# Kernel optimization log

Measured on AMD Instinct MI355X. Metric: run time of the kernel, lower is better.

Reference implementation:

```python
import jax, jax.numpy as jnp
import numpy as np

EPSILON = float(np.finfo(np.float32).tiny)
K = 64      # top-k edges to keep
TAU = 0.1   # gumbel-softmax temperature


def setup_inputs() -> dict:
    key = jax.random.key(0)
    k1, k2 = jax.random.split(key)
    B, N, E = 64, 256, 4
    scores = jax.random.normal(k1, (B, N, N, E), dtype=jnp.float32)
    # Gumbel(0,1) noise matching flat_scores shape [B*E, N*N]
    gumbel = jax.random.gumbel(k2, (B * E, N * N), dtype=jnp.float32)
    return {"scores": scores, "gumbel": gumbel}


def reference(scores, gumbel):
    B, N, _, E = scores.shape
    local_k = min(K, N * N)
    # [B, N, N, E] -> [B, E, N, N] -> [B*E, N*N]
    flat = scores.transpose(0, 3, 1, 2).reshape(B * E, N * N) + gumbel
    khot = jnp.zeros_like(flat)
    onehot = jnp.zeros_like(flat)

    def step(carry, _):
        flat, khot, onehot = carry
        khot_mask = jnp.maximum(1.0 - onehot, EPSILON)
        flat = flat + jnp.log(khot_mask)
        onehot = jax.nn.softmax(flat / TAU, axis=1)
        return (flat, khot + onehot, onehot), None

    (flat, khot, onehot), _ = jax.lax.scan(
        step, (flat, khot, onehot), None, length=local_k)

    # hard straight-through top-k
    _, ind = jax.lax.top_k(khot, local_k)                 # [B*E, local_k]
    rows = jnp.arange(khot.shape[0])[:, None]
    khot_hard = jnp.zeros_like(khot).at[rows, ind].set(1.0)
    res = khot_hard - jax.lax.stop_gradient(khot) + khot

    # [B*E, N*N] -> [B, E, N, N] -> [B, N, N, E]
    new_mask = res.reshape(B, E, N, N).transpose(0, 2, 3, 1)
    return new_mask
```

## Files before the change

kernel.cpp:

```cpp
#include <hip/hip_runtime.h>
#include <cfloat>

#define NROW   256
#define RLEN   65536
#define TPB    1024
#define VPT    64
#define REGS   8
#define MAXC   (TPB*REGS)
#define NITER  64
#define KSEL   64
#define THETA_OFF 8.0f
#define TCAP   256
#define LN_TGT 7.6246f

__global__ void __launch_bounds__(TPB)
GumbelSampler_2482491097709_kernel(const float* __restrict__ scores,
                                   const float* __restrict__ gumbel,
                                   float* __restrict__ out)
{
    __shared__ float s_A[16];
    __shared__ float s_B[16];
    __shared__ float s_EA[16];
    __shared__ float s_EB[16];
    __shared__ int   s_IC[16];
    __shared__ float s_mx[NITER];
    __shared__ float s_rcp[NITER];
    __shared__ int   s_cnt;
    __shared__ int   s_selB;
    __shared__ int   s_selR;
    __shared__ int   s_tcnt;
    __shared__ int   s_tie[TCAP];
    __shared__ int   s_hist[4096];
    __shared__ int   cand_idx[MAXC];
    __shared__ float cand_kv[MAXC];

    const int tid  = threadIdx.x;
    const int lane = tid & 63;
    const int wid  = tid >> 6;

    const int q    = blockIdx.x;
    const int xcd  = q & 7;
    const int slot = q >> 3;
    const int b    = xcd * 8 + (slot & 7);
    const int e    = slot >> 3;
    const int r    = b * 4 + e;

    const float* __restrict__ sr = scores + (size_t)b * (RLEN * 4) + e;
    const float* __restrict__ gr = gumbel + (size_t)r * RLEN;

    float v[VPT];
#pragma unroll
    for (int s = 0; s < VPT; ++s) {
        int p = tid + TPB * s;
        v[s] = sr[(size_t)p * 4] + gr[p];
    }

    float lm = -FLT_MAX;
#pragma unroll
    for (int s = 0; s < VPT; ++s) lm = fmaxf(lm, v[s]);
#pragma unroll
    for (int o = 32; o; o >>= 1) lm = fmaxf(lm, __shfl_xor(lm, o));
    if (lane == 0) s_A[wid] = lm;
    __syncthreads();
    float M0 = s_A[0];
#pragma unroll
    for (int w = 1; w < 16; ++w) M0 = fmaxf(M0, s_A[w]);
    const float C = M0 * 10.0f;

    float theta = M0 - THETA_OFF;
    for (int probe = 0; probe < 12; ++probe) {
        int lc = 0;
#pragma unroll
        for (int s = 0; s < VPT; ++s) lc += (v[s] >= theta) ? 1 : 0;
#pragma unroll
        for (int o = 32; o; o >>= 1) lc += __shfl_xor(lc, o);
        if (lane == 0) s_IC[wid] = lc;
        __syncthreads();
        int cc = 0;
#pragma unroll
        for (int w = 0; w < 16; ++w) cc += s_IC[w];
        __syncthreads();
        if (cc > MAXC - 64)      theta += __logf((float)cc) - LN_TGT;
        else if (cc < KSEL)      theta -= LN_TGT - __logf((float)(cc < 1 ? 1 : cc));
        else break;
    }

    if (tid == 0) s_cnt = 0;
    __syncthreads();
    {
        float mu = -FLT_MAX, u = 0.f;
#pragma unroll
        for (int s = 0; s < VPT; ++s) {
            float val = v[s];
            if (val >= theta) {
                int sl = atomicAdd(&s_cnt, 1);
                if (sl < MAXC) { cand_idx[sl] = tid + TPB * s; cand_kv[sl] = val; }
            } else {
                mu = fmaxf(mu, val);
                u += __expf(fmaf(val, 10.f, -C));
            }
        }
#pragma unroll
        for (int o = 32; o; o >>= 1) {
            mu = fmaxf(mu, __shfl_xor(mu, o));
            u += __shfl_xor(u, o);
        }
        if (lane == 0) { s_EA[wid] = mu; s_EB[wid] = u; }
    }
    __syncthreads();
    int cnt = s_cnt;
    float Mu = -FLT_MAX, U = 0.f;
#pragma unroll
    for (int w = 0; w < 16; ++w) { Mu = fmaxf(Mu, s_EA[w]); U += s_EB[w]; }

    float rcur[REGS];
#pragma unroll
    for (int j = 0; j < REGS; ++j) {
        int sl = tid + TPB * j;
        if (sl < cnt) {
            rcur[j] = cand_kv[sl];
            cand_kv[sl] = 0.f;
        } else rcur[j] = 0.f;
    }

    bool  noexp = false;
    float pmx = 0.f, prcp = 0.f, pt2 = 0.f;
    for (int t = 0; t < NITER; ++t) {
        float lmx = -FLT_MAX;
        if (t == 0) {
#pragma unroll
            for (int j = 0; j < REGS; ++j)
                if (tid + TPB * j < cnt) lmx = fmaxf(lmx, rcur[j]);
        } else {
#pragma unroll
            for (int j = 0; j < REGS; ++j) {
                int sl = tid + TPB * j;
                if (sl < cnt) {
                    float cur = rcur[j];
                    float y = fmaf(cur, 10.f, -pmx);
                    if (y > pt2) {
                        float o = __expf(y) * prcp;
                        cand_kv[sl] += o;
                        cur += __logf(fmaxf(1.f - o, FLT_MIN));
                        rcur[j] = cur;
                    }
                    lmx = fmaxf(lmx, cur);
                }
            }
        }
#pragma unroll
        for (int o = 32; o; o >>= 1) lmx = fmaxf(lmx, __shfl_xor(lmx, o));
        if (lane == 0) s_A[wid] = lmx;
        __syncthreads();
        float gm = s_A[0];
#pragma unroll
        for (int w = 1; w < 16; ++w) gm = fmaxf(gm, s_A[w]);
        const float mx = fmaxf(gm, Mu) * 10.f;

        float ls = 0.f;
#pragma unroll
        for (int j = 0; j < REGS; ++j)
            if (tid + TPB * j < cnt) ls += __expf(fmaf(rcur[j], 10.f, -mx));
#pragma unroll
        for (int o = 32; o; o >>= 1) ls += __shfl_xor(ls, o);
        if (lane == 0) s_B[wid] = ls;
        __syncthreads();
        float S = 0.f;
#pragma unroll
        for (int w = 0; w < 16; ++w) S += s_B[w];
        if (U > 0.f) S += __expf(C - mx + __logf(U));
        float lnse = __logf(S);
        float rcp  = 1.f / S;
        float t2   = lnse - 18.03f;
        if (tid == 0) { s_mx[t] = mx; s_rcp[t] = rcp; }
        pmx = mx; prcp = rcp; pt2 = t2;

        if (!noexp && t < NITER - 1) {
            float Lse = mx + lnse;
            if (10.f * Mu > Lse - 20.f) {
                float thOld = theta;
                float thN   = (Lse - 26.f) * 0.1f;
                int   oldc  = cnt;
                float mu2 = -FLT_MAX, u2 = 0.f;
#pragma unroll 4
                for (int s = 0; s < VPT; ++s) {
                    int p = tid + TPB * s;
                    float val = sr[(size_t)p * 4] + gr[p];
                    if (val < thOld) {
                        if (val >= thN) {
                            int sl = atomicAdd(&s_cnt, 1);
                            if (sl < MAXC) {
                                cand_idx[sl] = p;
                                cand_kv[sl]  = val;
                            }
                        } else {
                            mu2 = fmaxf(mu2, val);
                            u2 += __expf(fmaf(val, 10.f, -C));
                        }
                    }
                }
#pragma unroll
                for (int o = 32; o; o >>= 1) {
                    mu2 = fmaxf(mu2, __shfl_xor(mu2, o));
                    u2 += __shfl_xor(u2, o);
                }
                if (lane == 0) { s_EA[wid] = mu2; s_EB[wid] = u2; }
                __syncthreads();
                int newc = s_cnt;
                if (newc > MAXC) {
                    if (tid == 0) s_cnt = oldc;
                    noexp = true;
                } else {
                    float m2 = -FLT_MAX, uu = 0.f;
#pragma unroll
                    for (int w = 0; w < 16; ++w) {
                        m2 = fmaxf(m2, s_EA[w]); uu += s_EB[w];
                    }
                    Mu = m2; U = uu; theta = thN;
#pragma unroll
                    for (int j = 0; j < REGS; ++j) {
                        int sl = tid + TPB * j;
                        if (sl >= oldc && sl < newc) {
                            float vv = cand_kv[sl];
                            rcur[j] = vv;
                            float kb = 0.f;
                            for (int tt = 0; tt < t; ++tt)
                                kb += __expf(fmaf(vv, 10.f, -s_mx[tt])) * s_rcp[tt];
                            cand_kv[sl] = kb;
                        }
                    }
                    cnt = newc;
                }
            }
        }
    }
#pragma unroll
    for (int j = 0; j < REGS; ++j) {
        int sl = tid + TPB * j;
        if (sl < cnt) {
            float y = fmaf(rcur[j], 10.f, -pmx);
            if (y > pt2) cand_kv[sl] += __expf(y) * prcp;
        }
    }
    __syncthreads();

    unsigned prefix = 0;
    int Rrem = KSEL;
    for (int pass = 0; pass < 3; ++pass) {
        const int nbins = (pass == 2) ? 1024 : 2048;
        for (int i = tid; i < nbins; i += TPB) s_hist[i] = 0;
        __syncthreads();
#pragma unroll
        for (int j = 0; j < REGS; ++j) {
            int sl = tid + TPB * j;
            if (sl < cnt) {
                unsigned key = __float_as_uint(cand_kv[sl]);
                if (key != 0u) {
                    bool m; int bin;
                    if (pass == 0)      { m = true;                     bin = key >> 21; }
                    else if (pass == 1) { m = (key >> 21) == prefix;    bin = (key >> 10) & 2047; }
                    else                { m = (key >> 10) == prefix;    bin = key & 1023; }
                    if (m) atomicAdd(&s_hist[bin], 1);
                }
            }
        }
        __syncthreads();
        if (wid == 0) {
            int Rl = Rrem, found = -1;
            const int nch = nbins >> 6;
            for (int c = 0; c < nch && found < 0; ++c) {
                int bin = nbins - 1 - (c * 64 + lane);
                int h = s_hist[bin];
                int cum = h;
#pragma unroll
                for (int s2 = 1; s2 < 64; s2 <<= 1) {
                    int vv = __shfl_up(cum, s2);
                    if (lane >= s2) cum += vv;
                }
                unsigned long long mb = __ballot(cum >= Rl);
                if (mb) {
                    int fl = __ffsll(mb) - 1;
                    int cumex = __shfl(cum, fl) - __shfl(h, fl);
                    found = nbins - 1 - (c * 64 + fl);
                    Rl -= cumex;
                } else {
                    Rl -= __shfl(cum, 63);
                }
            }
            if (lane == 0) { s_selB = found; s_selR = Rl; }
        }
        __syncthreads();
        prefix = (prefix << ((pass == 2) ? 10 : 11)) | (unsigned)s_selB;
        Rrem = s_selR;
    }
    const unsigned Kstar = prefix;
    const int need = Rrem;

    if (tid == 0) s_tcnt = 0;
    __syncthreads();
#pragma unroll
    for (int j = 0; j < REGS; ++j) {
        int sl = tid + TPB * j;
        if (sl < cnt) {
            float kh = cand_kv[sl];
            unsigned key = __float_as_uint(kh);
            if (key > Kstar) {
                int p = cand_idx[sl];
                out[((size_t)b * RLEN + (size_t)p) * 4 + e] = (1.f - kh) + kh;
            } else if (key == Kstar) {
                int tp = atomicAdd(&s_tcnt, 1);
                if (tp < TCAP) s_tie[tp] = cand_idx[sl];
            }
        }
    }
    __syncthreads();
    if (wid == 0) {
        int T = s_tcnt < TCAP ? s_tcnt : TCAP;
        float kv = __uint_as_float(Kstar);
        float ov = (1.f - kv) + kv;
        for (int rdone = 0; rdone < need; ++rdone) {
            int bi = 0x7fffffff, bp = -1;
            for (int i = lane; i < T; i += 64) {
                int vv = s_tie[i];
                if (vv < bi) { bi = vv; bp = i; }
            }
#pragma unroll
            for (int s2 = 32; s2; s2 >>= 1) {
                int oi = __shfl_xor(bi, s2);
                int op = __shfl_xor(bp, s2);
                if (oi < bi) { bi = oi; bp = op; }
            }
            if (lane == 0 && bi != 0x7fffffff) {
                out[((size_t)b * RLEN + (size_t)bi) * 4 + e] = ov;
                s_tie[bp] = 0x7fffffff;
            }
        }
    }
}

extern "C" void kernel_launch(void* const* d_in, const int* in_sizes, int n_in,
                              void* d_out, int out_size, void* d_ws, size_t ws_size,
                              hipStream_t stream) {
    const float* scores = (const float*)d_in[0];
    const float* gumbel = (const float*)d_in[1];
    float* out = (float*)d_out;

    hipMemsetAsync(d_out, 0, (size_t)out_size * sizeof(float), stream);
    GumbelSampler_2482491097709_kernel<<<NROW, TPB, 0, stream>>>(scores, gumbel, out);
}
```

Measured before the change: 387.2 us.

## Fuse max and sum reductions per softmax iteration using lagged anchor

```diff
diff --git a/kernel.cpp b/kernel.cpp
--- a/kernel.cpp
+++ b/kernel.cpp
@@ -12,14 +12,16 @@
 #define THETA_OFF 8.0f
 #define TCAP   256
 #define LN_TGT 7.6246f
-
-__global__ void __launch_bounds__(TPB)
+#define AGUARD 40.0f
+
+__global__ void __launch_bounds__(TPB, 4)
 GumbelSampler_2482491097709_kernel(const float* __restrict__ scores,
                                    const float* __restrict__ gumbel,
                                    float* __restrict__ out)
 {
-    __shared__ float s_A[16];
-    __shared__ float s_B[16];
+    __shared__ float s_Am[2][16];
+    __shared__ float s_Bs[2][16];
+    __shared__ float s_R[16];
     __shared__ float s_EA[16];
     __shared__ float s_EB[16];
     __shared__ int   s_IC[16];
@@ -49,22 +51,24 @@
     const float* __restrict__ gr = gumbel + (size_t)r * RLEN;
 
     float v[VPT];
+    float lm = -FLT_MAX;
 #pragma unroll
     for (int s = 0; s < VPT; ++s) {
         int p = tid + TPB * s;
-        v[s] = sr[(size_t)p * 4] + gr[p];
-    }
-
-    float lm = -FLT_MAX;
-#pragma unroll
-    for (int s = 0; s < VPT; ++s) lm = fmaxf(lm, v[s]);
+        float x = sr[(size_t)p * 4] + gr[p];
+        v[s] = x;
+        lm = fmaxf(lm, x);
+    }
+#pragma unroll
+    for (int s = 0; s < VPT; ++s) asm volatile("" : "+v"(v[s]));
+
 #pragma unroll
     for (int o = 32; o; o >>= 1) lm = fmaxf(lm, __shfl_xor(lm, o));
-    if (lane == 0) s_A[wid] = lm;
-    __syncthreads();
-    float M0 = s_A[0];
-#pragma unroll
-    for (int w = 1; w < 16; ++w) M0 = fmaxf(M0, s_A[w]);
+    if (lane == 0) s_Am[0][wid] = lm;
+    __syncthreads();
+    float M0 = s_Am[0][0];
+#pragma unroll
+    for (int w = 1; w < 16; ++w) M0 = fmaxf(M0, s_Am[0][w]);
     const float C = M0 * 10.0f;
 
     float theta = M0 - THETA_OFF;
@@ -97,7 +101,8 @@
                 if (sl < MAXC) { cand_idx[sl] = tid + TPB * s; cand_kv[sl] = val; }
             } else {
                 mu = fmaxf(mu, val);
-                u += __expf(fmaf(val, 10.f, -C));
+                float yv = fmaf(val, 10.f, -C);
+                if (yv > -87.f) u += __expf(yv);
             }
         }
 #pragma unroll
@@ -124,20 +129,28 @@
     }
 
     bool  noexp = false;
-    float pmx = 0.f, prcp = 0.f, pt2 = 0.f;
+    float anc = C;
+    float pa = 0.f, prcp = 0.f, pt2 = 0.f;
     for (int t = 0; t < NITER; ++t) {
-        float lmx = -FLT_MAX;
+        const int pb = t & 1;
+        float lmx = -FLT_MAX, ls = 0.f;
         if (t == 0) {
-#pragma unroll
-            for (int j = 0; j < REGS; ++j)
-                if (tid + TPB * j < cnt) lmx = fmaxf(lmx, rcur[j]);
-        } else {
 #pragma unroll
             for (int j = 0; j < REGS; ++j) {
                 int sl = tid + TPB * j;
                 if (sl < cnt) {
                     float cur = rcur[j];
-                    float y = fmaf(cur, 10.f, -pmx);
+                    lmx = fmaxf(lmx, cur);
+                    ls += __expf(fmaf(cur, 10.f, -anc));
+                }
+            }
+        } else {
+#pragma unroll
+            for (int j = 0; j < REGS; ++j) {
+                int sl = tid + TPB * j;
+                if (sl < cnt) {
+                    float cur = rcur[j];
+                    float y = fmaf(cur, 10.f, -pa);
                     if (y > pt2) {
                         float o = __expf(y) * prcp;
                         cand_kv[sl] += o;
@@ -145,38 +158,58 @@
                         rcur[j] = cur;
                     }
                     lmx = fmaxf(lmx, cur);
-                }
-            }
-        }
-#pragma unroll
-        for (int o = 32; o; o >>= 1) lmx = fmaxf(lmx, __shfl_xor(lmx, o));
-        if (lane == 0) s_A[wid] = lmx;
-        __syncthreads();
-        float gm = s_A[0];
-#pragma unroll
-        for (int w = 1; w < 16; ++w) gm = fmaxf(gm, s_A[w]);
-        const float mx = fmaxf(gm, Mu) * 10.f;
-
-        float ls = 0.f;
-#pragma unroll
-        for (int j = 0; j < REGS; ++j)
-            if (tid + TPB * j < cnt) ls += __expf(fmaf(rcur[j], 10.f, -mx));
-#pragma unroll
-        for (int o = 32; o; o >>= 1) ls += __shfl_xor(ls, o);
-        if (lane == 0) s_B[wid] = ls;
-        __syncthreads();
-        float S = 0.f;
-#pragma unroll
-        for (int w = 0; w < 16; ++w) S += s_B[w];
-        if (U > 0.f) S += __expf(C - mx + __logf(U));
+                    ls += __expf(fmaf(cur, 10.f, -anc));
+                }
+            }
+        }
+#pragma unroll
+        for (int o = 32; o; o >>= 1) {
+            lmx = fmaxf(lmx, __shfl_xor(lmx, o));
+            ls += __shfl_xor(ls, o);
+        }
+        if (lane == 0) { s_Am[pb][wid] = lmx; s_Bs[pb][wid] = ls; }
+        __syncthreads();
+        float gm, Ssum;
+        {
+            const float4* pA = (const float4*)&s_Am[pb][0];
+            const float4* pB = (const float4*)&s_Bs[pb][0];
+            float4 a0 = pA[0], a1 = pA[1], a2 = pA[2], a3 = pA[3];
+            float4 b0 = pB[0], b1 = pB[1], b2 = pB[2], b3 = pB[3];
+            gm = fmaxf(fmaxf(fmaxf(a0.x, a0.y), fmaxf(a0.z, a0.w)),
+                 fmaxf(fmaxf(fmaxf(a1.x, a1.y), fmaxf(a1.z, a1.w)),
+                 fmaxf(fmaxf(fmaxf(a2.x, a2.y), fmaxf(a2.z, a2.w)),
+                       fmaxf(fmaxf(a3.x, a3.y), fmaxf(a3.z, a3.w)))));
+            Ssum = ((b0.x + b0.y) + (b0.z + b0.w))
+                 + ((b1.x + b1.y) + (b1.z + b1.w))
+                 + ((b2.x + b2.y) + (b2.z + b2.w))
+                 + ((b3.x + b3.y) + (b3.z + b3.w));
+        }
+        float anext = fmaxf(gm, Mu) * 10.f;
+        float aeff  = anc;
+        float S     = Ssum;
+        if (anc - anext > AGUARD) {
+            float l2 = 0.f;
+#pragma unroll
+            for (int j = 0; j < REGS; ++j)
+                if (tid + TPB * j < cnt) l2 += __expf(fmaf(rcur[j], 10.f, -anext));
+#pragma unroll
+            for (int o = 32; o; o >>= 1) l2 += __shfl_xor(l2, o);
+            if (lane == 0) s_R[wid] = l2;
+            __syncthreads();
+            S = 0.f;
+#pragma unroll
+            for (int w = 0; w < 16; ++w) S += s_R[w];
+            aeff = anext;
+        }
+        if (U > 0.f) S += __expf(C - aeff + __logf(U));
         float lnse = __logf(S);
         float rcp  = 1.f / S;
-        float t2   = lnse - 18.03f;
-        if (tid == 0) { s_mx[t] = mx; s_rcp[t] = rcp; }
-        pmx = mx; prcp = rcp; pt2 = t2;
+        if (tid == 0) { s_mx[t] = aeff; s_rcp[t] = rcp; }
+        pa = aeff; prcp = rcp; pt2 = lnse - 18.03f;
+        anc = anext;
 
         if (!noexp && t < NITER - 1) {
-            float Lse = mx + lnse;
+            float Lse = aeff + lnse;
             if (10.f * Mu > Lse - 20.f) {
                 float thOld = theta;
                 float thN   = (Lse - 26.f) * 0.1f;
@@ -195,7 +228,8 @@
                             }
                         } else {
                             mu2 = fmaxf(mu2, val);
-                            u2 += __expf(fmaf(val, 10.f, -C));
+                            float yv = fmaf(val, 10.f, -C);
+                            if (yv > -87.f) u2 += __expf(yv);
                         }
                     }
                 }
@@ -238,7 +272,7 @@
     for (int j = 0; j < REGS; ++j) {
         int sl = tid + TPB * j;
         if (sl < cnt) {
-            float y = fmaf(rcur[j], 10.f, -pmx);
+            float y = fmaf(rcur[j], 10.f, -pa);
             if (y > pt2) cand_kv[sl] += __expf(y) * prcp;
         }
     }
```

Result: faster. 369.7 us (-4.5%).

## Anchor softmax on previous log-sum-exp to drop per-iteration max reduction

Applied to the files above, without the earlier changes.

```diff
diff --git a/kernel.cpp b/kernel.cpp
--- a/kernel.cpp
+++ b/kernel.cpp
@@ -12,19 +12,18 @@
 #define THETA_OFF 8.0f
 #define TCAP   256
 #define LN_TGT 7.6246f
-
-__global__ void __launch_bounds__(TPB)
+#define GATE  (-18.03f)
+
+__global__ void __launch_bounds__(TPB, 4)
 GumbelSampler_2482491097709_kernel(const float* __restrict__ scores,
                                    const float* __restrict__ gumbel,
                                    float* __restrict__ out)
 {
-    __shared__ float s_A[16];
-    __shared__ float s_B[16];
+    __shared__ float s_P[2][16];
     __shared__ float s_EA[16];
     __shared__ float s_EB[16];
     __shared__ int   s_IC[16];
-    __shared__ float s_mx[NITER];
-    __shared__ float s_rcp[NITER];
+    __shared__ float s_Lse[NITER];
     __shared__ int   s_cnt;
     __shared__ int   s_selB;
     __shared__ int   s_selR;
@@ -49,22 +48,24 @@
     const float* __restrict__ gr = gumbel + (size_t)r * RLEN;
 
     float v[VPT];
+    float lm = -FLT_MAX;
 #pragma unroll
     for (int s = 0; s < VPT; ++s) {
         int p = tid + TPB * s;
-        v[s] = sr[(size_t)p * 4] + gr[p];
-    }
-
-    float lm = -FLT_MAX;
-#pragma unroll
-    for (int s = 0; s < VPT; ++s) lm = fmaxf(lm, v[s]);
+        float x = sr[(size_t)p * 4] + gr[p];
+        v[s] = x;
+        lm = fmaxf(lm, x);
+    }
+#pragma unroll
+    for (int s = 0; s < VPT; ++s) asm volatile("" : "+v"(v[s]));
+
 #pragma unroll
     for (int o = 32; o; o >>= 1) lm = fmaxf(lm, __shfl_xor(lm, o));
-    if (lane == 0) s_A[wid] = lm;
-    __syncthreads();
-    float M0 = s_A[0];
-#pragma unroll
-    for (int w = 1; w < 16; ++w) M0 = fmaxf(M0, s_A[w]);
+    if (lane == 0) s_P[0][wid] = lm;
+    __syncthreads();
+    float M0 = s_P[0][lane & 15];
+#pragma unroll
+    for (int o = 8; o; o >>= 1) M0 = fmaxf(M0, __shfl_xor(M0, o));
     const float C = M0 * 10.0f;
 
     float theta = M0 - THETA_OFF;
@@ -76,9 +77,9 @@
         for (int o = 32; o; o >>= 1) lc += __shfl_xor(lc, o);
         if (lane == 0) s_IC[wid] = lc;
         __syncthreads();
-        int cc = 0;
-#pragma unroll
-        for (int w = 0; w < 16; ++w) cc += s_IC[w];
+        int cc = s_IC[lane & 15];
+#pragma unroll
+        for (int o = 8; o; o >>= 1) cc += __shfl_xor(cc, o);
         __syncthreads();
         if (cc > MAXC - 64)      theta += __logf((float)cc) - LN_TGT;
         else if (cc < KSEL)      theta -= LN_TGT - __logf((float)(cc < 1 ? 1 : cc));
@@ -92,12 +93,19 @@
 #pragma unroll
         for (int s = 0; s < VPT; ++s) {
             float val = v[s];
-            if (val >= theta) {
-                int sl = atomicAdd(&s_cnt, 1);
+            bool pr = (val >= theta);
+            unsigned long long m = __ballot(pr);
+            if (pr) {
+                int lead = __ffsll(m) - 1;
+                int base = 0;
+                if (lane == lead) base = atomicAdd(&s_cnt, (int)__popcll(m));
+                base = __shfl(base, lead);
+                int sl = base + (int)__popcll(m & ((1ull << lane) - 1ull));
                 if (sl < MAXC) { cand_idx[sl] = tid + TPB * s; cand_kv[sl] = val; }
             } else {
                 mu = fmaxf(mu, val);
-                u += __expf(fmaf(val, 10.f, -C));
+                float yv = fmaf(val, 10.f, -C);
+                if (yv > -87.f) u += __expf(yv);
             }
         }
 #pragma unroll
@@ -109,9 +117,12 @@
     }
     __syncthreads();
     int cnt = s_cnt;
-    float Mu = -FLT_MAX, U = 0.f;
-#pragma unroll
-    for (int w = 0; w < 16; ++w) { Mu = fmaxf(Mu, s_EA[w]); U += s_EB[w]; }
+    float Mu = s_EA[lane & 15], U = s_EB[lane & 15];
+#pragma unroll
+    for (int o = 8; o; o >>= 1) {
+        Mu = fmaxf(Mu, __shfl_xor(Mu, o));
+        U += __shfl_xor(U, o);
+    }
 
     float rcur[REGS];
 #pragma unroll
@@ -124,122 +135,109 @@
     }
 
     bool  noexp = false;
-    float pmx = 0.f, prcp = 0.f, pt2 = 0.f;
+    float anc = C;
     for (int t = 0; t < NITER; ++t) {
-        float lmx = -FLT_MAX;
+        const int pb = t & 1;
+        float ls = 0.f;
         if (t == 0) {
 #pragma unroll
             for (int j = 0; j < REGS; ++j)
-                if (tid + TPB * j < cnt) lmx = fmaxf(lmx, rcur[j]);
+                if (tid + TPB * j < cnt)
+                    ls += __expf(fmaf(rcur[j], 10.f, -anc));
         } else {
 #pragma unroll
             for (int j = 0; j < REGS; ++j) {
                 int sl = tid + TPB * j;
                 if (sl < cnt) {
                     float cur = rcur[j];
-                    float y = fmaf(cur, 10.f, -pmx);
-                    if (y > pt2) {
-                        float o = __expf(y) * prcp;
-                        cand_kv[sl] += o;
-                        cur += __logf(fmaxf(1.f - o, FLT_MIN));
+                    float y = fmaf(cur, 10.f, -anc);
+                    float e_ = __expf(y);
+                    if (y > GATE) {
+                        cand_kv[sl] += e_;
+                        cur += __logf(fmaxf(1.f - e_, FLT_MIN));
                         rcur[j] = cur;
+                        e_ = __expf(fmaf(cur, 10.f, -anc));
                     }
-                    lmx = fmaxf(lmx, cur);
-                }
-            }
-        }
-#pragma unroll
-        for (int o = 32; o; o >>= 1) lmx = fmaxf(lmx, __shfl_xor(lmx, o));
-        if (lane == 0) s_A[wid] = lmx;
-        __syncthreads();
-        float gm = s_A[0];
-#pragma unroll
-        for (int w = 1; w < 16; ++w) gm = fmaxf(gm, s_A[w]);
-        const float mx = fmaxf(gm, Mu) * 10.f;
-
-        float ls = 0.f;
-#pragma unroll
-        for (int j = 0; j < REGS; ++j)
-            if (tid + TPB * j < cnt) ls += __expf(fmaf(rcur[j], 10.f, -mx));
+                    ls += e_;
+                }
+            }
+        }
 #pragma unroll
         for (int o = 32; o; o >>= 1) ls += __shfl_xor(ls, o);
-        if (lane == 0) s_B[wid] = ls;
-        __syncthreads();
-        float S = 0.f;
-#pragma unroll
-        for (int w = 0; w < 16; ++w) S += s_B[w];
-        if (U > 0.f) S += __expf(C - mx + __logf(U));
-        float lnse = __logf(S);
-        float rcp  = 1.f / S;
-        float t2   = lnse - 18.03f;
-        if (tid == 0) { s_mx[t] = mx; s_rcp[t] = rcp; }
-        pmx = mx; prcp = rcp; pt2 = t2;
-
-        if (!noexp && t < NITER - 1) {
-            float Lse = mx + lnse;
-            if (10.f * Mu > Lse - 20.f) {
-                float thOld = theta;
-                float thN   = (Lse - 26.f) * 0.1f;
-                int   oldc  = cnt;
-                float mu2 = -FLT_MAX, u2 = 0.f;
+        if (lane == 0) s_P[pb][wid] = ls;
+        __syncthreads();
+        float S = s_P[pb][lane & 15];
+#pragma unroll
+        for (int o = 8; o; o >>= 1) S += __shfl_xor(S, o);
+        if (U > 0.f) S += __expf(C - anc + __logf(U));
+        float Lse = anc + __logf(S);
+        if (tid == 0) s_Lse[t] = Lse;
+
+        if (!noexp && t < NITER - 1 && 10.f * Mu > Lse - 20.f) {
+            float thOld = theta;
+            float thN   = (Lse - 26.f) * 0.1f;
+            int   oldc  = cnt;
+            float mu2 = -FLT_MAX, u2 = 0.f;
 #pragma unroll 4
-                for (int s = 0; s < VPT; ++s) {
-                    int p = tid + TPB * s;
-                    float val = sr[(size_t)p * 4] + gr[p];
-                    if (val < thOld) {
-                        if (val >= thN) {
-                            int sl = atomicAdd(&s_cnt, 1);
-                            if (sl < MAXC) {
-                                cand_idx[sl] = p;
-                                cand_kv[sl]  = val;
-                            }
-                        } else {
-                            mu2 = fmaxf(mu2, val);
-                            u2 += __expf(fmaf(val, 10.f, -C));
+            for (int s = 0; s < VPT; ++s) {
+                int p = tid + TPB * s;
+                float val = sr[(size_t)p * 4] + gr[p];
+                if (val < thOld) {
+                    if (val >= thN) {
+                        int sl = atomicAdd(&s_cnt, 1);
+                        if (sl < MAXC) {
+                            cand_idx[sl] = p;
+                            cand_kv[sl]  = val;
                         }
+                    } else {
+                        mu2 = fmaxf(mu2, val);
+                        float yv = fmaf(val, 10.f, -C);
+                        if (yv > -87.f) u2 += __expf(yv);
                     }
                 }
-#pragma unroll
-                for (int o = 32; o; o >>= 1) {
-                    mu2 = fmaxf(mu2, __shfl_xor(mu2, o));
-                    u2 += __shfl_xor(u2, o);
-                }
-                if (lane == 0) { s_EA[wid] = mu2; s_EB[wid] = u2; }
-                __syncthreads();
-                int newc = s_cnt;
-                if (newc > MAXC) {
-                    if (tid == 0) s_cnt = oldc;
-                    noexp = true;
-                } else {
-                    float m2 = -FLT_MAX, uu = 0.f;
-#pragma unroll
-                    for (int w = 0; w < 16; ++w) {
-                        m2 = fmaxf(m2, s_EA[w]); uu += s_EB[w];
+            }
+#pragma unroll
+            for (int o = 32; o; o >>= 1) {
+                mu2 = fmaxf(mu2, __shfl_xor(mu2, o));
+                u2 += __shfl_xor(u2, o);
+            }
+            if (lane == 0) { s_EA[wid] = mu2; s_EB[wid] = u2; }
+            __syncthreads();
+            int newc = s_cnt;
+            if (newc > MAXC) {
+                if (tid == 0) s_cnt = oldc;
+                noexp = true;
+            } else {
+                float m2 = s_EA[lane & 15], uu = s_EB[lane & 15];
+#pragma unroll
+                for (int o = 8; o; o >>= 1) {
+                    m2 = fmaxf(m2, __shfl_xor(m2, o));
+                    uu += __shfl_xor(uu, o);
+                }
+                Mu = m2; U = uu; theta = thN;
+#pragma unroll
+                for (int j = 0; j < REGS; ++j) {
+                    int sl = tid + TPB * j;
+                    if (sl >= oldc && sl < newc) {
+                        float vv = cand_kv[sl];
+                        rcur[j] = vv;
+                        float kb = 0.f;
+                        for (int tt = 0; tt < t; ++tt)
+                            kb += __expf(fmaf(vv, 10.f, -s_Lse[tt]));
+                        cand_kv[sl] = kb;
                     }
-                    Mu = m2; U = uu; theta = thN;
-#pragma unroll
-                    for (int j = 0; j < REGS; ++j) {
-                        int sl = tid + TPB * j;
-                        if (sl >= oldc && sl < newc) {
-                            float vv = cand_kv[sl];
-                            rcur[j] = vv;
-                            float kb = 0.f;
-                            for (int tt = 0; tt < t; ++tt)
-                                kb += __expf(fmaf(vv, 10.f, -s_mx[tt])) * s_rcp[tt];
-                            cand_kv[sl] = kb;
-                        }
-                    }
-                    cnt = newc;
-                }
-            }
-        }
+                }
+                cnt = newc;
+            }
+        }
+        anc = Lse;
     }
 #pragma unroll
     for (int j = 0; j < REGS; ++j) {
         int sl = tid + TPB * j;
         if (sl < cnt) {
-            float y = fmaf(rcur[j], 10.f, -pmx);
-            if (y > pt2) cand_kv[sl] += __expf(y) * prcp;
+            float y = fmaf(rcur[j], 10.f, -anc);
+            if (y > GATE) cand_kv[sl] += __expf(y);
         }
     }
     __syncthreads();
@@ -268,7 +266,8 @@
         if (wid == 0) {
             int Rl = Rrem, found = -1;
             const int nch = nbins >> 6;
-            for (int c = 0; c < nch && found < 0; ++c) {
+            const int c0 = (pass == 0) ? 23 : 0;
+            for (int c = c0; c < nch && found < 0; ++c) {
                 int bin = nbins - 1 - (c * 64 + lane);
                 int h = s_hist[bin];
                 int cum = h;
```

After: 343.7 us. 11.2% less time.
